# Kernel optimization log

Measured on AMD Instinct MI355X. Metric: run time of the kernel, lower is better.

The kernel has to match this reference:

```python
import jax, jax.numpy as jnp
import numpy as np
from math import sqrt

B = 32          # batch
C = 81          # label_num (class 0 = background, skipped)
N = 15130       # number of default boxes
K = 200         # max_num candidates per class
MAX_OUT = 200   # max_output boxes per image
SCORE_THR = 0.05
CRITERIA = 0.45
SCALE_XY = 0.1
SCALE_WH = 0.2
NEG_INF = -1e30


def make_dboxes_xywh():
    """Replicates DefaultBoxes for figsize (1200,1200), SSD-R34 COCO config."""
    fig = 1200
    feat = [50, 25, 13, 7, 3, 3]
    scales = [int(s * fig / 300) for s in [21, 45, 99, 153, 207, 261, 315]]
    aspect_ratios = [[2], [2, 3], [2, 3], [2, 3], [2], [2]]
    boxes = []
    for idx, f in enumerate(feat):
        step = int(fig / f)
        fk = fig // step  # == f for this config
        sk1 = scales[idx] / fig
        sk2 = scales[idx + 1] / fig
        sk3 = sqrt(sk1 * sk2)
        sizes = [(sk1, sk1), (sk3, sk3)]
        for a in aspect_ratios[idx]:
            w, h = sk1 * sqrt(a), sk1 / sqrt(a)
            sizes.append((w, h))
            sizes.append((h, w))
        for (w, h) in sizes:
            for i in range(f):
                for j in range(f):
                    cx, cy = (j + 0.5) / fk, (i + 0.5) / fk
                    boxes.append((cx, cy, w, h))
    d = np.clip(np.array(boxes, dtype=np.float32), 0.0, 1.0)
    assert d.shape[0] == N
    return d[None, :, :]  # [1, N, 4]


def setup_inputs() -> dict:
    key = jax.random.key(0)
    k1, k2 = jax.random.split(key)
    bboxes_in = jax.random.normal(k1, (B, 4, N), dtype=jnp.float32)
    scores_in = jax.random.normal(k2, (B, C, N), dtype=jnp.float32)
    dboxes_xywh = jnp.asarray(make_dboxes_xywh())
    return {"bboxes_in": bboxes_in, "scores_in": scores_in, "dboxes_xywh": dboxes_xywh}


def scale_back_batch(bboxes_in, scores_in, dboxes_xywh):
    b = jnp.transpose(bboxes_in, (0, 2, 1))            # [B, N, 4]
    xy = SCALE_XY * b[..., :2] * dboxes_xywh[..., 2:] + dboxes_xywh[..., :2]
    wh = jnp.exp(SCALE_WH * b[..., 2:]) * dboxes_xywh[..., 2:]
    ltrb = jnp.concatenate([xy - 0.5 * wh, xy + 0.5 * wh], axis=-1)  # [B, N, 4]
    probs = jax.nn.softmax(jnp.transpose(scores_in, (0, 2, 1)), axis=-1)  # [B, N, C]
    return ltrb, probs


def pairwise_iou(b):
    """Faithful to calc_iou_tensor: the masked_fill_ on delta.clone() is a no-op
    in the original, so negative deltas are NOT clamped."""
    lt = jnp.maximum(b[:, None, :2], b[None, :, :2])
    rb = jnp.minimum(b[:, None, 2:], b[None, :, 2:])
    d = rb - lt
    inter = d[..., 0] * d[..., 1]
    area = (b[:, 2] - b[:, 0]) * (b[:, 3] - b[:, 1])
    return inter / (area[:, None] + area[None, :] - inter)  # [K, K]


def nms_one_class(boxes, score):
    """boxes [N,4], score [N] -> kept boxes [K,4], kept scores [K] (NEG_INF = dropped).
    Greedy NMS over the top-K scores in descending order, matching the original
    while-loop (ascending sort + pop-from-end)."""
    s = jnp.where(score > SCORE_THR, score, NEG_INF)
    top_s, top_i = jax.lax.top_k(s, K)         # descending
    bk = boxes[top_i]                          # [K, 4]
    iou = pairwise_iou(bk)                     # [K, K]
    rng = jnp.arange(K)
    keep0 = top_s > NEG_INF

    def body(i, keep):
        suppress = keep[i] & (iou[i] >= CRITERIA) & (rng > i)
        return keep & ~suppress

    keep = jax.lax.fori_loop(0, K, body, keep0)
    return bk, jnp.where(keep, top_s, NEG_INF)


def decode_image(boxes, probs):
    """boxes [N,4], probs [N,C] -> (boxes [MAX_OUT,4], labels [MAX_OUT], scores [MAX_OUT])."""
    cls_scores = jnp.transpose(probs[:, 1:])                    # [C-1, N] (skip background)
    bks, ss = jax.vmap(nms_one_class, in_axes=(None, 0))(boxes, cls_scores)  # [C-1,K,4],[C-1,K]
    labels = jnp.repeat(jnp.arange(1, C, dtype=jnp.int32), K)   # [(C-1)*K]
    flat_s = ss.reshape(-1)
    top_s, top_i = jax.lax.top_k(flat_s, MAX_OUT)               # global top max_output
    out_boxes = bks.reshape(-1, 4)[top_i]
    out_labels = labels[top_i]
    valid = top_s > NEG_INF
    return (jnp.where(valid[:, None], out_boxes, 0.0),
            jnp.where(valid, out_labels, 0),
            jnp.where(valid, top_s, 0.0))


def reference(bboxes_in, scores_in, dboxes_xywh):
    ltrb, probs = scale_back_batch(bboxes_in, scores_in, dboxes_xywh)
    boxes, labels, scores = jax.vmap(decode_image)(ltrb, probs)
    return boxes, labels, scores  # [B,MAX_OUT,4], [B,MAX_OUT] int32, [B,MAX_OUT]
```

## Files before the change

kernel.cpp:

```cpp
#include <hip/hip_runtime.h>
#include <cstdint>
#include <cstddef>

#define BATCH 32
#define NCLS 81
#define NFG 80
#define NBOX 15130
#define NCHUNK 60
#define TOPK 200
#define NTASK (BATCH * NFG)
#define NEG_INF -1e30f
#define GCAP 1024
#define SORTCAP 1024
#define LCAP 1920
#define SCORE_THR 0.05f
#define CRITERIA 0.45f

__global__ __launch_bounds__(256) void k1_fused(
    const float* __restrict__ bboxes,
    const float* __restrict__ scores,
    const float* __restrict__ dboxes,
    float4* __restrict__ ltrb,
    unsigned long long* __restrict__ gcand,
    int* __restrict__ gcnt)
{
    const int blk = blockIdx.x;
    const int b = blk / NCHUNK;
    const int chunk = blk - b * NCHUNK;
    const int tid = threadIdx.x;
    const int n = chunk * 256 + tid;

    __shared__ unsigned long long list[LCAP];
    __shared__ int lcnt;
    __shared__ int ccnt[NFG];
    __shared__ int cbase[NFG];

    if (tid == 0) lcnt = 0;
    if (tid < NFG) ccnt[tid] = 0;
    __syncthreads();

    float m = 0.f, s = 1.f, thrv = 1e30f;
    const float* sc = scores;

    if (n < NBOX) {
        const float* bb = bboxes + (size_t)b * 4 * NBOX + n;
        float bx = bb[0];
        float by = bb[NBOX];
        float bw = bb[2 * (size_t)NBOX];
        float bh = bb[3 * (size_t)NBOX];
        float4 d = reinterpret_cast<const float4*>(dboxes)[n];
        float xx = __fadd_rn(__fmul_rn(__fmul_rn(0.1f, bx), d.z), d.x);
        float yy = __fadd_rn(__fmul_rn(__fmul_rn(0.1f, by), d.w), d.y);
        float wx = __fmul_rn(expf(__fmul_rn(0.2f, bw)), d.z);
        float wy = __fmul_rn(expf(__fmul_rn(0.2f, bh)), d.w);
        float4 o;
        o.x = __fsub_rn(xx, __fmul_rn(0.5f, wx));
        o.y = __fsub_rn(yy, __fmul_rn(0.5f, wy));
        o.z = __fadd_rn(xx, __fmul_rn(0.5f, wx));
        o.w = __fadd_rn(yy, __fmul_rn(0.5f, wy));
        ltrb[(size_t)b * NBOX + n] = o;

        sc = scores + (size_t)b * NCLS * NBOX + n;
        {
            float vals[NCLS];
#pragma unroll
            for (int c = 0; c < NCLS; ++c) vals[c] = sc[(size_t)c * NBOX];
            m = vals[0];
#pragma unroll
            for (int c = 1; c < NCLS; ++c) m = fmaxf(m, vals[c]);
            float ss = 0.0f;
#pragma unroll
            for (int c = 0; c < NCLS; ++c) ss = __fadd_rn(ss, expf(__fsub_rn(vals[c], m)));
            s = ss;
        }
        thrv = __fsub_rn(__fadd_rn(m, logf(__fmul_rn(0.05f, s))), 1e-3f);
    }

    if (n < NBOX) {
        uintptr_t scu = (uintptr_t)sc;
        asm volatile("" : "+v"(scu));
        const float* scv = (const float*)scu;
        for (int c0 = 1; c0 < NCLS; c0 += 16) {
            float vt[16];
#pragma unroll
            for (int u = 0; u < 16; ++u) {
                int c = c0 + u;
                vt[u] = (c < NCLS) ? scv[(size_t)c * NBOX] : -1e30f;
            }
#pragma unroll
            for (int u = 0; u < 16; ++u) {
                int c = c0 + u;
                if (vt[u] > thrv) {
                    float p = __fdiv_rn(expf(__fsub_rn(vt[u], m)), s);
                    if (p > SCORE_THR) {
                        int e = atomicAdd(&lcnt, 1);
                        if (e < LCAP) {
                            list[e] = ((unsigned long long)__float_as_uint(p) << 32) |
                                      ((unsigned long long)(unsigned)(c - 1) << 24) |
                                      (unsigned long long)(unsigned)n;
                        } else {
                            int pos = atomicAdd(&gcnt[b * NFG + (c - 1)], 1);
                            if (pos < GCAP)
                                gcand[(size_t)(b * NFG + (c - 1)) * GCAP + pos] =
                                    ((unsigned long long)__float_as_uint(p) << 32) |
                                    (unsigned long long)(0xFFFFFFFFu - (unsigned)n);
                        }
                    }
                }
            }
        }
    }
    __syncthreads();

    const int E = min(lcnt, LCAP);

    for (int i = tid; i < E; i += 256) {
        int c = (int)((list[i] >> 24) & 0xFF);
        atomicAdd(&ccnt[c], 1);
    }
    __syncthreads();

    if (tid < NFG && ccnt[tid] > 0)
        cbase[tid] = atomicAdd(&gcnt[b * NFG + tid], ccnt[tid]);
    __syncthreads();
    if (tid < NFG) ccnt[tid] = 0;
    __syncthreads();

    for (int i = tid; i < E; i += 256) {
        unsigned long long e = list[i];
        int c = (int)((e >> 24) & 0xFF);
        unsigned nn = (unsigned)(e & 0xFFFFFF);
        int pos = cbase[c] + atomicAdd(&ccnt[c], 1);
        if (pos < GCAP) {
            unsigned pb = (unsigned)(e >> 32);
            gcand[(size_t)(b * NFG + c) * GCAP + pos] =
                ((unsigned long long)pb << 32) |
                (unsigned long long)(0xFFFFFFFFu - nn);
        }
    }
}

template<int NR, int J, int K>
__device__ __forceinline__ void bstep(unsigned long long (&it)[NR], const int lane) {
    if constexpr (J >= 64) {
        constexpr int M = J >> 6;
#pragma unroll
        for (int r = 0; r < NR; ++r) {
            const int rp = r ^ M;
            if (rp > r) {
                const bool desc = (((unsigned)(r << 6) & (unsigned)K) == 0u);
                unsigned long long a = it[r], bb = it[rp];
                if (desc ? (a < bb) : (a > bb)) { it[r] = bb; it[rp] = a; }
            }
        }
    } else {
#pragma unroll
        for (int r = 0; r < NR; ++r) {
            unsigned long long a = it[r];
            unsigned long long bb = __shfl_xor(a, J, 64);
            const unsigned i = ((unsigned)(r << 6)) | (unsigned)lane;
            const bool desc = ((i & (unsigned)K) == 0u);
            const bool lower = ((lane & J) == 0);
            it[r] = ((desc == lower) ? (a >= bb) : (a <= bb)) ? a : bb;
        }
    }
}

template<int NR, int K, int J>
__device__ __forceinline__ void bstage(unsigned long long (&it)[NR], const int lane) {
    bstep<NR, J, K>(it, lane);
    if constexpr (J > 1) bstage<NR, K, (J >> 1)>(it, lane);
}

template<int NR>
__device__ __forceinline__ void bsort(unsigned long long (&it)[NR], const int lane,
                                      const unsigned kmax) {
    bstage<NR, 2, 1>(it, lane);
    if (kmax >= 4)   bstage<NR, 4, 2>(it, lane);
    if (kmax >= 8)   bstage<NR, 8, 4>(it, lane);
    if (kmax >= 16)  bstage<NR, 16, 8>(it, lane);
    if (kmax >= 32)  bstage<NR, 32, 16>(it, lane);
    if (kmax >= 64)  bstage<NR, 64, 32>(it, lane);
    if constexpr (NR >= 4) {
        if (kmax >= 128) bstage<NR, 128, 64>(it, lane);
        if (kmax >= 256) bstage<NR, 256, 128>(it, lane);
    }
    if constexpr (NR >= 8)  { if (kmax >= 512)  bstage<NR, 512, 256>(it, lane); }
    if constexpr (NR >= 16) { if (kmax >= 1024) bstage<NR, 1024, 512>(it, lane); }
}

__global__ __launch_bounds__(64) void k2_nms(
    const unsigned long long* __restrict__ gcand,
    const int* __restrict__ gcnt,
    const float4* __restrict__ ltrb,
    float* __restrict__ cls_scores,
    int* __restrict__ cls_idx)
{
    const int t = blockIdx.x;
    const int b = t / NFG;
    const int lane = threadIdx.x;

    __shared__ float4 sbox[TOPK];
    __shared__ float sarea[TOPK];

    const int cl = min(gcnt[t], SORTCAP);
    const unsigned long long* gc = gcand + (size_t)t * GCAP;

    unsigned kmax = 2;
    while (kmax < (unsigned)cl) kmax <<= 1;

    unsigned long long top4[4];
    if (cl <= 256) {
        unsigned long long it[4];
#pragma unroll
        for (int r = 0; r < 4; ++r) {
            const int i = (r << 6) + lane;
            it[r] = (i < cl) ? gc[i] : 0ULL;
        }
        bsort<4>(it, lane, kmax);
#pragma unroll
        for (int r = 0; r < 4; ++r) top4[r] = it[r];
    } else if (cl <= 512) {
        unsigned long long it[8];
#pragma unroll
        for (int r = 0; r < 8; ++r) {
            const int i = (r << 6) + lane;
            it[r] = (i < cl) ? gc[i] : 0ULL;
        }
        bsort<8>(it, lane, kmax);
#pragma unroll
        for (int r = 0; r < 4; ++r) top4[r] = it[r];
    } else {
        unsigned long long it[16];
#pragma unroll
        for (int r = 0; r < 16; ++r) {
            const int i = (r << 6) + lane;
            it[r] = (i < cl) ? gc[i] : 0ULL;
        }
        bsort<16>(it, lane, kmax);
#pragma unroll
        for (int r = 0; r < 4; ++r) top4[r] = it[r];
    }

    const int mk = min(cl, TOPK);

    float4 myb[4];
    float mya[4], myp[4];
    int myn[4];
#pragma unroll
    for (int r = 0; r < 4; ++r) {
        const int i = (r << 6) + lane;
        myb[r] = make_float4(0.f, 0.f, 0.f, 0.f);
        mya[r] = 0.f; myp[r] = 0.f; myn[r] = 0;
        if (i < mk) {
            const unsigned long long key = top4[r];
            const unsigned n = 0xFFFFFFFFu - (unsigned)(key & 0xFFFFFFFFull);
            const float4 bx = ltrb[(size_t)b * NBOX + n];
            myb[r] = bx;
            mya[r] = __fmul_rn(__fsub_rn(bx.z, bx.x), __fsub_rn(bx.w, bx.y));
            myp[r] = __uint_as_float((unsigned)(key >> 32));
            myn[r] = b * NBOX + (int)n;
            sbox[i] = bx;
            sarea[i] = mya[r];
        }
    }
    __syncthreads();

    auto maskBits = [](int r) -> unsigned long long {
        if (r <= 0) return 0ULL;
        if (r >= 64) return ~0ULL;
        return (1ULL << r) - 1ULL;
    };
    unsigned long long kw0 = maskBits(mk);
    unsigned long long kw1 = maskBits(mk - 64);
    unsigned long long kw2 = maskBits(mk - 128);
    unsigned long long kw3 = maskBits(mk - 192);

    float4 nb = sbox[0];
    float na = sarea[0];

#define NMS_QUAD(KWQ, Q)                                                           \
    {                                                                              \
        const int i0 = (Q) << 6;                                                   \
        const int i1 = min(mk, i0 + 64);                                           \
        for (int i = i0; i < i1; ++i) {                                            \
            const float4 bi = nb;                                                  \
            const float ai = na;                                                   \
            const int ip = min(i + 1, TOPK - 1);                                   \
            nb = sbox[ip];                                                         \
            na = sarea[ip];                                                        \
            if ((KWQ >> (i - i0)) & 1ULL) {                                        \
                _Pragma("unroll")                                                  \
                for (int q2 = 0; q2 < 4; ++q2) {                                   \
                    const int j = (q2 << 6) + lane;                                \
                    const float4 bj = myb[q2];                                     \
                    const float ltx = fmaxf(bi.x, bj.x), lty = fmaxf(bi.y, bj.y);  \
                    const float rbx = fminf(bi.z, bj.z), rby = fminf(bi.w, bj.w);  \
                    const float dx = __fsub_rn(rbx, ltx), dy = __fsub_rn(rby, lty);\
                    const float inter = __fmul_rn(dx, dy);                         \
                    const float uni = __fsub_rn(__fadd_rn(ai, mya[q2]), inter);    \
                    const float iou = __fdiv_rn(inter, uni);                       \
                    const unsigned long long sup =                                 \
                        __ballot((iou >= CRITERIA) && (j > i));                    \
                    if (q2 == 0) kw0 &= ~sup;                                      \
                    else if (q2 == 1) kw1 &= ~sup;                                 \
                    else if (q2 == 2) kw2 &= ~sup;                                 \
                    else kw3 &= ~sup;                                              \
                }                                                                  \
            }                                                                      \
        }                                                                          \
    }
    NMS_QUAD(kw0, 0)
    NMS_QUAD(kw1, 1)
    NMS_QUAD(kw2, 2)
    NMS_QUAD(kw3, 3)
#undef NMS_QUAD

#pragma unroll
    for (int r = 0; r < 4; ++r) {
        const int i = (r << 6) + lane;
        if (i < TOPK) {
            const unsigned long long kq = (r == 0) ? kw0 : (r == 1) ? kw1
                                         : (r == 2) ? kw2 : kw3;
            const bool keep = (i < mk) && ((kq >> lane) & 1ULL);
            cls_scores[(size_t)t * TOPK + i] = keep ? myp[r] : NEG_INF;
            if (i < mk) cls_idx[(size_t)t * TOPK + i] = myn[r];
        }
    }
}

__device__ __forceinline__ int blockReduceSum(int x, int* red, int tid) {
    __syncthreads();
    red[tid] = x;
    __syncthreads();
    for (int off = 128; off > 0; off >>= 1) {
        if (tid < off) red[tid] += red[tid + off];
        __syncthreads();
    }
    return red[0];
}

__global__ __launch_bounds__(256) void k3_topk(
    const float* __restrict__ cls_scores,
    const int* __restrict__ cls_idx,
    const float4* __restrict__ ltrb,
    float* __restrict__ out)
{
    const int b = blockIdx.x;
    const int tid = threadIdx.x;
    const int NFLAT = NFG * TOPK;
    const int PER = 63;

    __shared__ unsigned long long sel[512];
    __shared__ int scnt;
    __shared__ int red[256];

    const float* S = cls_scores + (size_t)b * NFLAT;
    float v[PER];
#pragma unroll
    for (int i = 0; i < PER; ++i) {
        int j = i * 256 + tid;
        v[i] = (j < NFLAT) ? S[j] : NEG_INF;
    }

    int lc = 0;
#pragma unroll
    for (int i = 0; i < PER; ++i) lc += (v[i] > -1e29f) ? 1 : 0;
    int validCount = blockReduceSum(lc, red, tid);

    unsigned thrBits = 0;
    if (validCount > TOPK) {
        unsigned lo = 0, hi = 0x7F800000u;
        while (lo < hi) {
            unsigned mid = (lo + hi) >> 1;
            float mf = __uint_as_float(mid);
            int c2 = 0;
#pragma unroll
            for (int i = 0; i < PER; ++i) c2 += (v[i] > mf) ? 1 : 0;
            int tot = blockReduceSum(c2, red, tid);
            if (tot < TOPK) hi = mid; else lo = mid + 1;
        }
        thrBits = lo;
    }

    __syncthreads();
    if (tid == 0) scnt = 0;
    for (int i = tid; i < 512; i += 256) sel[i] = 0ULL;
    __syncthreads();

    const bool useGE = (validCount > TOPK);
    const float thrF = __uint_as_float(thrBits);
#pragma unroll
    for (int i = 0; i < PER; ++i) {
        int j = i * 256 + tid;
        bool take = useGE ? (v[i] >= thrF) : (v[i] > -1e29f);
        if (j < NFLAT && take) {
            int pos = atomicAdd(&scnt, 1);
            if (pos < 512) {
                sel[pos] = ((unsigned long long)__float_as_uint(v[i]) << 32) |
                           (unsigned long long)(0xFFFFFFFFu - (unsigned)j);
            }
        }
    }
    __syncthreads();
    int total = min(min(scnt, 512), TOPK);

    for (unsigned k = 2; k <= 512; k <<= 1) {
        for (unsigned j = k >> 1; j > 0; j >>= 1) {
            for (unsigned i = tid; i < 512; i += 256) {
                unsigned ixj = i ^ j;
                if (ixj > i) {
                    unsigned long long a = sel[i], bb2 = sel[ixj];
                    bool desc = ((i & k) == 0);
                    if (desc ? (a < bb2) : (a > bb2)) { sel[i] = bb2; sel[ixj] = a; }
                }
            }
            __syncthreads();
        }
    }

    if (tid < TOPK) {
        size_t ob = (size_t)b * TOPK + tid;
        float4 bx = make_float4(0.f, 0.f, 0.f, 0.f);
        float lab = 0.f, sc2 = 0.f;
        if (tid < total) {
            unsigned long long key = sel[tid];
            unsigned j = 0xFFFFFFFFu - (unsigned)(key & 0xFFFFFFFFull);
            sc2 = __uint_as_float((unsigned)(key >> 32));
            unsigned cls = j / TOPK;
            int gi = cls_idx[(size_t)b * NFLAT + j];
            bx = ltrb[gi];
            lab = (float)(cls + 1);
        }
        reinterpret_cast<float4*>(out)[ob] = bx;
        out[(size_t)BATCH * TOPK * 4 + ob] = lab;
        out[(size_t)BATCH * TOPK * 4 + (size_t)BATCH * TOPK + ob] = sc2;
    }
}

extern "C" void kernel_launch(void* const* d_in, const int* in_sizes, int n_in,
                              void* d_out, int out_size, void* d_ws, size_t ws_size,
                              hipStream_t stream) {
    (void)in_sizes; (void)n_in; (void)out_size; (void)ws_size;
    const float* bboxes = (const float*)d_in[0];
    const float* scores = (const float*)d_in[1];
    const float* dboxes = (const float*)d_in[2];
    float* out = (float*)d_out;

    char* ws = (char*)d_ws;
    size_t off = 0;
    float4* ltrb = (float4*)(ws + off);      off += (size_t)BATCH * NBOX * 16;
    unsigned long long* gcand = (unsigned long long*)(ws + off);
                                             off += (size_t)NTASK * GCAP * 8;
    float* cls_scores = (float*)(ws + off);  off += (size_t)NTASK * TOPK * 4;
    int*   cls_idx    = (int*)(ws + off);    off += (size_t)NTASK * TOPK * 4;
    int*   gcnt       = (int*)(ws + off);    off += (size_t)NTASK * 4;

    hipMemsetAsync(gcnt, 0, NTASK * sizeof(int), stream);

    k1_fused<<<BATCH * NCHUNK, 256, 0, stream>>>(bboxes, scores, dboxes, ltrb, gcand, gcnt);
    k2_nms<<<NTASK, 64, 0, stream>>>(gcand, gcnt, ltrb, cls_scores, cls_idx);
    k3_topk<<<BATCH, 256, 0, stream>>>(cls_scores, cls_idx, ltrb, out);
}
```

Baseline: 209.1 us.

## Stage class scores into LDS via direct global-to-LDS loads in k1

The fused softmax/candidate kernel now stages each block's 81x128 score tile into shared memory with global_load_lds, instead of reading every score twice from global memory through registers. Blocks shrink from 256 to 128 threads and the grid grows to 119 chunks per image, with the local candidate list capacity reduced to fit the new LDS budget. This removes the second global pass over the scores and the large register array, at the cost of about 41KB of LDS per block, which may limit occupancy. The smaller LCAP also sends more candidates down the global atomic fallback path.

```diff
diff --git a/kernel.cpp b/kernel.cpp
--- a/kernel.cpp
+++ b/kernel.cpp
@@ -6,17 +6,18 @@
 #define NCLS 81
 #define NFG 80
 #define NBOX 15130
-#define NCHUNK 60
+#define TW 128
+#define NCHUNK3 119
 #define TOPK 200
 #define NTASK (BATCH * NFG)
 #define NEG_INF -1e30f
 #define GCAP 1024
 #define SORTCAP 1024
-#define LCAP 1920
+#define LCAP 768
 #define SCORE_THR 0.05f
 #define CRITERIA 0.45f
 
-__global__ __launch_bounds__(256) void k1_fused(
+__global__ __launch_bounds__(128) void k1_fused(
     const float* __restrict__ bboxes,
     const float* __restrict__ scores,
     const float* __restrict__ dboxes,
@@ -25,11 +26,16 @@
     int* __restrict__ gcnt)
 {
     const int blk = blockIdx.x;
-    const int b = blk / NCHUNK;
-    const int chunk = blk - b * NCHUNK;
+    const int b = blk / NCHUNK3;
+    const int chunk = blk - b * NCHUNK3;
     const int tid = threadIdx.x;
-    const int n = chunk * 256 + tid;
-
+    const int lane = tid & 63;
+    const int w = tid >> 6;
+    const int nbase = chunk * TW;
+    const int n = nbase + tid;
+    const bool valid = (n < NBOX);
+
+    __shared__ float tile[NCLS][TW];
     __shared__ unsigned long long list[LCAP];
     __shared__ int lcnt;
     __shared__ int ccnt[NFG];
@@ -37,12 +43,8 @@
 
     if (tid == 0) lcnt = 0;
     if (tid < NFG) ccnt[tid] = 0;
-    __syncthreads();
-
-    float m = 0.f, s = 1.f, thrv = 1e30f;
-    const float* sc = scores;
-
-    if (n < NBOX) {
+
+    if (valid) {
         const float* bb = bboxes + (size_t)b * 4 * NBOX + n;
         float bx = bb[0];
         float by = bb[NBOX];
@@ -59,52 +61,53 @@
         o.z = __fadd_rn(xx, __fmul_rn(0.5f, wx));
         o.w = __fadd_rn(yy, __fmul_rn(0.5f, wy));
         ltrb[(size_t)b * NBOX + n] = o;
-
-        sc = scores + (size_t)b * NCLS * NBOX + n;
-        {
-            float vals[NCLS];
-#pragma unroll
-            for (int c = 0; c < NCLS; ++c) vals[c] = sc[(size_t)c * NBOX];
-            m = vals[0];
-#pragma unroll
-            for (int c = 1; c < NCLS; ++c) m = fmaxf(m, vals[c]);
-            float ss = 0.0f;
-#pragma unroll
-            for (int c = 0; c < NCLS; ++c) ss = __fadd_rn(ss, expf(__fsub_rn(vals[c], m)));
-            s = ss;
-        }
-        thrv = __fsub_rn(__fadd_rn(m, logf(__fmul_rn(0.05f, s))), 1e-3f);
-    }
-
-    if (n < NBOX) {
-        uintptr_t scu = (uintptr_t)sc;
-        asm volatile("" : "+v"(scu));
-        const float* scv = (const float*)scu;
-        for (int c0 = 1; c0 < NCLS; c0 += 16) {
-            float vt[16];
-#pragma unroll
-            for (int u = 0; u < 16; ++u) {
-                int c = c0 + u;
-                vt[u] = (c < NCLS) ? scv[(size_t)c * NBOX] : -1e30f;
+    }
+
+    {
+        const float* gp = scores + (size_t)b * NCLS * NBOX + nbase + (w << 6) + lane;
+        if (nbase + (w << 6) + lane < NBOX) {
+#pragma unroll
+            for (int c = 0; c < NCLS; ++c) {
+                __builtin_amdgcn_global_load_lds(
+                    (const void*)(gp + (size_t)c * NBOX),
+                    (void*)&tile[c][w << 6], 4, 0, 0);
             }
-#pragma unroll
-            for (int u = 0; u < 16; ++u) {
-                int c = c0 + u;
-                if (vt[u] > thrv) {
-                    float p = __fdiv_rn(expf(__fsub_rn(vt[u], m)), s);
-                    if (p > SCORE_THR) {
-                        int e = atomicAdd(&lcnt, 1);
-                        if (e < LCAP) {
-                            list[e] = ((unsigned long long)__float_as_uint(p) << 32) |
-                                      ((unsigned long long)(unsigned)(c - 1) << 24) |
-                                      (unsigned long long)(unsigned)n;
-                        } else {
-                            int pos = atomicAdd(&gcnt[b * NFG + (c - 1)], 1);
-                            if (pos < GCAP)
-                                gcand[(size_t)(b * NFG + (c - 1)) * GCAP + pos] =
-                                    ((unsigned long long)__float_as_uint(p) << 32) |
-                                    (unsigned long long)(0xFFFFFFFFu - (unsigned)n);
-                        }
+        }
+    }
+    __syncthreads();
+
+    float m = -INFINITY, ssum = 1.f, thrv = 1e30f;
+    if (valid) {
+        float mm = tile[0][tid];
+#pragma unroll
+        for (int c = 1; c < NCLS; ++c) mm = fmaxf(mm, tile[c][tid]);
+        m = mm;
+        float ss = 0.0f;
+#pragma unroll
+        for (int c = 0; c < NCLS; ++c)
+            ss = __fadd_rn(ss, expf(__fsub_rn(tile[c][tid], m)));
+        ssum = ss;
+        thrv = __fsub_rn(__fadd_rn(m, logf(__fmul_rn(0.05f, ssum))), 1e-3f);
+    }
+
+    if (valid) {
+#pragma unroll
+        for (int c = 1; c < NCLS; ++c) {
+            float v = tile[c][tid];
+            if (v > thrv) {
+                float p = __fdiv_rn(expf(__fsub_rn(v, m)), ssum);
+                if (p > SCORE_THR) {
+                    int e = atomicAdd(&lcnt, 1);
+                    if (e < LCAP) {
+                        list[e] = ((unsigned long long)__float_as_uint(p) << 32) |
+                                  ((unsigned long long)(unsigned)(c - 1) << 24) |
+                                  (unsigned long long)(unsigned)n;
+                    } else {
+                        int pos = atomicAdd(&gcnt[b * NFG + (c - 1)], 1);
+                        if (pos < GCAP)
+                            gcand[(size_t)(b * NFG + (c - 1)) * GCAP + pos] =
+                                ((unsigned long long)__float_as_uint(p) << 32) |
+                                (unsigned long long)(0xFFFFFFFFu - (unsigned)n);
                     }
                 }
             }
@@ -114,7 +117,7 @@
 
     const int E = min(lcnt, LCAP);
 
-    for (int i = tid; i < E; i += 256) {
+    for (int i = tid; i < E; i += TW) {
         int c = (int)((list[i] >> 24) & 0xFF);
         atomicAdd(&ccnt[c], 1);
     }
@@ -126,7 +129,7 @@
     if (tid < NFG) ccnt[tid] = 0;
     __syncthreads();
 
-    for (int i = tid; i < E; i += 256) {
+    for (int i = tid; i < E; i += TW) {
         unsigned long long e = list[i];
         int c = (int)((e >> 24) & 0xFF);
         unsigned nn = (unsigned)(e & 0xFFFFFF);
@@ -458,7 +461,7 @@
 
     hipMemsetAsync(gcnt, 0, NTASK * sizeof(int), stream);
 
-    k1_fused<<<BATCH * NCHUNK, 256, 0, stream>>>(bboxes, scores, dboxes, ltrb, gcand, gcnt);
+    k1_fused<<<BATCH * NCHUNK3, TW, 0, stream>>>(bboxes, scores, dboxes, ltrb, gcand, gcnt);
     k2_nms<<<NTASK, 64, 0, stream>>>(gcand, gcnt, ltrb, cls_scores, cls_idx);
     k3_topk<<<BATCH, 256, 0, stream>>>(cls_scores, cls_idx, ltrb, out);
 }
```

New measurement: 269.7 us. +29.0%, slower.
